# Performance work log

Hardware: AMD Instinct MI355X
Metric: run time of the kernel (lower is better)

## Reference

```python
import jax, jax.numpy as jnp
import numpy as np

B, I, H = 16384, 512, 512


def setup_inputs() -> dict:
    key = jax.random.key(0)
    ks = jax.random.split(key, 6)
    scale_s = 1.0 / np.sqrt(H + I + 1)
    scale_g = 1.0 / np.sqrt(H + I + H)
    return {
        "x_t": jax.random.normal(ks[0], (B, I), dtype=jnp.float32),
        "delta_t": jax.random.uniform(ks[1], (B, 1), dtype=jnp.float32),
        "h_prev": jax.random.normal(ks[2], (B, H), dtype=jnp.float32),
        "c_prev": jax.random.normal(ks[3], (B, H), dtype=jnp.float32),
        # linear_s: in = H + I + 1
        "Ws": jax.random.normal(ks[4], (H + I + 1, H), dtype=jnp.float32) * scale_s,
        "bs": jnp.zeros((H,), dtype=jnp.float32),
        # stacked weights for the 5 gates (f, i, T, u, o), each in = H + I + H
        "Wg": jax.random.normal(ks[5], (2 * H + I, 5 * H), dtype=jnp.float32) * scale_g,
        "bg": jnp.zeros((5 * H,), dtype=jnp.float32),
    }


def reference(x_t, delta_t, h_prev, c_prev, Ws, bs, Wg, bg):
    # time gate: s_t = tanh(Linear([h_prev, x_t, delta_t]))
    s_t = jnp.tanh(jnp.concatenate([h_prev, x_t, delta_t], axis=1) @ Ws + bs)
    # shared-input GEMM for the 5 gates on concat([h_prev, x_t, s_t])
    z = jnp.concatenate([h_prev, x_t, s_t], axis=1) @ Wg + bg  # [B, 5H]
    f_t = jax.nn.sigmoid(z[:, 0 * H:1 * H])
    i_t = jax.nn.sigmoid(z[:, 1 * H:2 * H])
    T_t = jax.nn.sigmoid(z[:, 2 * H:3 * H])
    zeta_t = jnp.tanh(z[:, 3 * H:4 * H])
    o_t = jax.nn.sigmoid(z[:, 4 * H:5 * H])
    c_t = f_t * c_prev + i_t * zeta_t + T_t * s_t
    h_t = o_t * jnp.tanh(c_t)
    return (h_t, c_t)
```

## Files before the change

### kernel.cpp

```cpp
#include <hip/hip_runtime.h>
#include <stdint.h>
#include <stddef.h>

#define Bsz 16384
#define Hsz 512
#define KG 1536
#define KA 1024
#define NT2 24

typedef float f32x4 __attribute__((ext_vector_type(4)));
typedef short bf16x8 __attribute__((ext_vector_type(8)));
typedef unsigned short u16;
typedef unsigned int u32;

__device__ __forceinline__ u16 f2bf(float f) {
  union { float f; unsigned u; } v; v.f = f;
  return (u16)((v.u + 0x7fffu + ((v.u >> 16) & 1u)) >> 16);
}
__device__ __forceinline__ float bf2f(u16 h) {
  union { unsigned u; float f; } v; v.u = ((unsigned)h) << 16;
  return v.f;
}
__device__ __forceinline__ float sigm(float x) {
  return 1.0f / (1.0f + __expf(-x));
}
__device__ __forceinline__ float tanh_(float x) {
  x = fminf(fmaxf(x, -15.0f), 15.0f);
  float e = __expf(2.0f * x);
  return (e - 1.0f) / (e + 1.0f);
}

__device__ __forceinline__ void gload_lds16(const u16* g, u16* l) {
  __builtin_amdgcn_global_load_lds(
      (__attribute__((address_space(1))) void*)(g),
      (__attribute__((address_space(3))) void*)(l), 16, 0, 0);
}

#define VMCNT(n) asm volatile("s_waitcnt vmcnt(" #n ")" ::: "memory")
#define BAR() { asm volatile("" ::: "memory"); __builtin_amdgcn_s_barrier(); \
                asm volatile("" ::: "memory"); }

__global__ __launch_bounds__(256) void prep_A_kernel(
    const float* __restrict__ h_prev, const float* __restrict__ x_t,
    u16* __restrict__ A) {
  const int b = blockIdx.x;
  const int q = threadIdx.x;
  const int qq = q & 127;
  const float4* src = (q < 128) ? (const float4*)h_prev : (const float4*)x_t;
  float4 v = src[(size_t)b * 128 + qq];
  ushort4 o;
  o.x = f2bf(v.x); o.y = f2bf(v.y); o.z = f2bf(v.z); o.w = f2bf(v.w);
  *(ushort4*)(A + (size_t)b * KG + (size_t)q * 4) = o;
}

__global__ __launch_bounds__(256) void transpose_cast_kernel(
    const float* __restrict__ in, u16* __restrict__ out, int R, int C) {
  __shared__ float tile[32][33];
  const int c0 = blockIdx.x * 32;
  const int r0 = blockIdx.y * 32;
  const int tx = threadIdx.x;
  const int ty = threadIdx.y;
  #pragma unroll
  for (int i = ty; i < 32; i += 8)
    tile[i][tx] = in[(size_t)(r0 + i) * C + (c0 + tx)];
  __syncthreads();
  #pragma unroll
  for (int i = ty; i < 32; i += 8)
    out[(size_t)(c0 + i) * R + (r0 + tx)] = f2bf(tile[tx][i]);
}

__global__ __launch_bounds__(256, 2) void gemm1_kernel(
    const u16* __restrict__ A, const u16* __restrict__ Wst,
    const float* __restrict__ Ws, const float* __restrict__ bs,
    const float* __restrict__ delta, u16* __restrict__ Aout) {
  __shared__ __attribute__((aligned(16))) u16 Als[128][32];
  __shared__ __attribute__((aligned(16))) u16 Bls[128][32];
  const int t = threadIdx.x;
  const int w = t >> 6, l = t & 63;
  const int bm0 = blockIdx.y * 128;
  const int bn0 = blockIdx.x * 128;
  const int wm = w >> 1, wn = w & 1;

  f32x4 zv = {0.f, 0.f, 0.f, 0.f};
  f32x4 acc[4][4];
  #pragma unroll
  for (int i = 0; i < 4; ++i)
    #pragma unroll
    for (int j = 0; j < 4; ++j) acc[i][j] = zv;

  const int r = t >> 2, q = t & 3;
  const u16* gA0 = A + (size_t)(bm0 + r) * KG + q * 8;
  const u16* gA1 = A + (size_t)(bm0 + 64 + r) * KG + q * 8;
  const u16* gB0 = Wst + (size_t)(bn0 + r) * KA + q * 8;
  const u16* gB1 = Wst + (size_t)(bn0 + 64 + r) * KA + q * 8;
  u16* lA0 = &Als[0][0] + w * 512;
  u16* lA1 = &Als[0][0] + 2048 + w * 512;
  u16* lB0 = &Bls[0][0] + w * 512;
  u16* lB1 = &Bls[0][0] + 2048 + w * 512;

  const int frow = l & 15;
  const int kofs = (l >> 4) * 8;

  for (int kt = 0; kt < KA / 32; ++kt) {
    const int ko = kt * 32;
    gload_lds16(gA0 + ko, lA0);
    gload_lds16(gA1 + ko, lA1);
    gload_lds16(gB0 + ko, lB0);
    gload_lds16(gB1 + ko, lB1);
    __syncthreads();
    bf16x8 af[4], bfv[4];
    #pragma unroll
    for (int mi = 0; mi < 4; ++mi)
      af[mi] = *(const bf16x8*)&Als[wm * 64 + mi * 16 + frow][kofs];
    #pragma unroll
    for (int ni = 0; ni < 4; ++ni)
      bfv[ni] = *(const bf16x8*)&Bls[wn * 64 + ni * 16 + frow][kofs];
    #pragma unroll
    for (int mi = 0; mi < 4; ++mi)
      #pragma unroll
      for (int ni = 0; ni < 4; ++ni)
        acc[mi][ni] = __builtin_amdgcn_mfma_f32_16x16x32_bf16(
            af[mi], bfv[ni], acc[mi][ni], 0, 0, 0);
    __syncthreads();
  }

  #pragma unroll
  for (int ni = 0; ni < 4; ++ni) {
    const int col = bn0 + wn * 64 + ni * 16 + (l & 15);
    const float wsl = Ws[(size_t)1024 * 512 + col];
    const float bsv = bs[col];
    #pragma unroll
    for (int mi = 0; mi < 4; ++mi) {
      #pragma unroll
      for (int rr = 0; rr < 4; ++rr) {
        const int row = bm0 + wm * 64 + mi * 16 + (l >> 4) * 4 + rr;
        const float z = acc[mi][ni][rr] + delta[row] * wsl + bsv;
        Aout[(size_t)row * KG + 1024 + col] = f2bf(tanh_(z));
      }
    }
  }
}

__global__ __launch_bounds__(512, 2) void gemm2_8ph(
    const u16* __restrict__ A, const u16* __restrict__ Wgt,
    const float* __restrict__ bg, const float* __restrict__ c_prev,
    float* __restrict__ out) {
  __shared__ __attribute__((aligned(16))) u16 LDSA[2][256 * 64];
  __shared__ __attribute__((aligned(16))) u16 LDSB[2][320 * 64];

  const int t5 = threadIdx.x;
  const int w = t5 >> 6;
  const int l = t5 & 63;

  const int bid = blockIdx.x;
  const int hb = bid & 7;
  const int rb = bid >> 3;
  const int bm0 = rb * 256;
  const int h0 = hb * 64;

  const bool isA = (w < 4);

  const int lrow = l >> 3, lch = l & 7;
  const size_t laneoff = (size_t)lrow * KG + (size_t)((lch ^ lrow) * 8);

  const u16* gbase = isA ? (A + (size_t)(bm0 + w * 64) * KG + laneoff)
                         : (Wgt + (size_t)h0 * KG + laneoff);
  u32 boff[10];
  #pragma unroll
  for (int s = 0; s < 10; ++s) {
    int rB = (w - 4) * 80 + s * 8;
    boff[s] = (u32)(((rB >> 6) * Hsz + (rB & 63)) * KG);
  }

#define STAGE(kt) { const u32 _ko = (u32)(kt) * 64; const int _b = (kt) & 1; \
    if (isA) { \
      u16* lb = &LDSA[_b][0] + w * 4096; \
      _Pragma("unroll") \
      for (int s = 0; s < 8; ++s) \
        gload_lds16(gbase + _ko + s * (8 * KG), lb + s * 512); \
    } else { \
      u16* lb = &LDSB[_b][0] + (w - 4) * 5120; \
      _Pragma("unroll") \
      for (int s = 0; s < 10; ++s) \
        gload_lds16(gbase + _ko + boff[s], lb + s * 512); \
    } }

  f32x4 zv = {0.f, 0.f, 0.f, 0.f};
  f32x4 acc[8][5];
  #pragma unroll
  for (int mi = 0; mi < 8; ++mi)
    #pragma unroll
    for (int g = 0; g < 5; ++g) acc[mi][g] = zv;

  const int wm = w >> 2;
  const int wn = w & 3;
  const int frow = l & 15;
  const int kq = l >> 4;
  const int f7 = frow & 7;
  const u32 abase  = (u32)((wm * 128 + frow) * 64 + ((kq ^ f7) * 8));
  const u32 bbase  = (u32)((wn * 16 + frow) * 64 + ((kq ^ f7) * 8));
  const u32 abase2 = abase ^ 32;
  const u32 bbase2 = bbase ^ 32;

#define LDA4(Asrc, off) { af[0] = *(const bf16x8*)&Asrc[(off)]; \
    af[1] = *(const bf16x8*)&Asrc[(off) + 1024]; \
    af[2] = *(const bf16x8*)&Asrc[(off) + 2048]; \
    af[3] = *(const bf16x8*)&Asrc[(off) + 3072]; }
#define LDB5(Bsrc, off) { bfv[0] = *(const bf16x8*)&Bsrc[(off)]; \
    bfv[1] = *(const bf16x8*)&Bsrc[(off) + 4096]; \
    bfv[2] = *(const bf16x8*)&Bsrc[(off) + 8192]; \
    bfv[3] = *(const bf16x8*)&Bsrc[(off) + 12288]; \
    bfv[4] = *(const bf16x8*)&Bsrc[(off) + 16384]; }
#define MFMA20(base) { __builtin_amdgcn_s_setprio(1); \
    _Pragma("unroll") \
    for (int g = 0; g < 5; ++g) { \
      _Pragma("unroll") \
      for (int mi = 0; mi < 4; ++mi) \
        acc[(base) + mi][g] = __builtin_amdgcn_mfma_f32_16x16x32_bf16( \
            af[mi], bfv[g], acc[(base) + mi][g], 0, 0, 0); \
    } \
    __builtin_amdgcn_s_setprio(0); }

  STAGE(0) STAGE(1)

  for (int t = 0; t < NT2; ++t) {
    const int rem = NT2 - 1 - t;
    if (rem >= 1) { VMCNT(8); } else { VMCNT(0); }
    BAR();
    const u16* As = &LDSA[t & 1][0];
    const u16* Bs = &LDSB[t & 1][0];
    bf16x8 af[4], bfv[5];
    LDA4(As, abase) LDB5(Bs, bbase)
    MFMA20(0)
    BAR();
    LDA4(As, abase + 4096)
    MFMA20(4)
    BAR();
    LDA4(As, abase2) LDB5(Bs, bbase2)
    MFMA20(0)
    BAR();
    LDA4(As, abase2 + 4096)
    MFMA20(4)
    BAR();
    if (rem >= 2) STAGE(t + 2)
  }
#undef STAGE

  const int hc = h0 + wn * 16 + frow;
  const float b_f = bg[hc];
  const float b_i = bg[Hsz + hc];
  const float b_T = bg[2 * Hsz + hc];
  const float b_z = bg[3 * Hsz + hc];
  const float b_o = bg[4 * Hsz + hc];
  #pragma unroll
  for (int mi = 0; mi < 8; ++mi) {
    #pragma unroll
    for (int rr = 0; rr < 4; ++rr) {
      const int row = bm0 + wm * 128 + mi * 16 + kq * 4 + rr;
      const float fg = sigm(acc[mi][0][rr] + b_f);
      const float ig = sigm(acc[mi][1][rr] + b_i);
      const float Tg = sigm(acc[mi][2][rr] + b_T);
      const float zg = tanh_(acc[mi][3][rr] + b_z);
      const float og = sigm(acc[mi][4][rr] + b_o);
      const float cp = c_prev[(size_t)row * Hsz + hc];
      const float st = bf2f(A[(size_t)row * KG + 1024 + hc]);
      const float c = fg * cp + ig * zg + Tg * st;
      const float h = og * tanh_(c);
      out[(size_t)row * Hsz + hc] = h;
      out[(size_t)Bsz * Hsz + (size_t)row * Hsz + hc] = c;
    }
  }
}

extern "C" void kernel_launch(void* const* d_in, const int* in_sizes, int n_in,
                              void* d_out, int out_size, void* d_ws, size_t ws_size,
                              hipStream_t stream) {
  const float* x_t    = (const float*)d_in[0];
  const float* delta  = (const float*)d_in[1];
  const float* h_prev = (const float*)d_in[2];
  const float* c_prev = (const float*)d_in[3];
  const float* Ws     = (const float*)d_in[4];
  const float* bs     = (const float*)d_in[5];
  const float* Wg     = (const float*)d_in[6];
  const float* bg     = (const float*)d_in[7];
  float* out = (float*)d_out;

  char* wsb = (char*)d_ws;
  u16* A   = (u16*)(wsb);
  u16* Wst = (u16*)(wsb + (size_t)50331648);
  u16* Wgt = (u16*)(wsb + (size_t)51380224);

  prep_A_kernel<<<dim3(16384), dim3(256), 0, stream>>>(h_prev, x_t, A);
  transpose_cast_kernel<<<dim3(16, 32), dim3(32, 8), 0, stream>>>(Ws, Wst, 1024, 512);
  transpose_cast_kernel<<<dim3(80, 48), dim3(32, 8), 0, stream>>>(Wg, Wgt, 1536, 2560);
  gemm1_kernel<<<dim3(4, 128), dim3(256), 0, stream>>>(A, Wst, Ws, bs, delta, A);
  gemm2_8ph<<<dim3(512), dim3(512), 0, stream>>>(A, Wgt, bg, c_prev, out);
}
```

Before: 211.4 us.

## Load gate-weight fragments directly into registers and triple-buffer A tiles in LDS

The gate GEMM no longer stages the weight tile in shared memory. Each wave loads its B fragments straight from global memory into registers, double-buffered across k-steps. The A tile now uses a three-deep LDS ring with 32-wide k-steps. Inline ds_read plus lgkmcnt waits interleave fragment reads with MFMAs, and there are fewer barriers per step. This removes LDS traffic and LDS capacity for B, but it adds redundant global/L2 reads of the weights across waves and more register pressure.

```diff
diff --git a/kernel.cpp b/kernel.cpp
--- a/kernel.cpp
+++ b/kernel.cpp
@@ -6,7 +6,7 @@
 #define Hsz 512
 #define KG 1536
 #define KA 1024
-#define NT2 24
+#define NT3 48
 
 typedef float f32x4 __attribute__((ext_vector_type(4)));
 typedef short bf16x8 __attribute__((ext_vector_type(8)));
@@ -36,7 +36,15 @@
       (__attribute__((address_space(3))) void*)(l), 16, 0, 0);
 }
 
+__device__ __forceinline__ bf16x8 ds_read128(u32 byte_addr) {
+  bf16x8 r;
+  asm volatile("ds_read_b128 %0, %1" : "=v"(r) : "v"(byte_addr));
+  return r;
+}
+
 #define VMCNT(n) asm volatile("s_waitcnt vmcnt(" #n ")" ::: "memory")
+#define LGKM(n) { asm volatile("s_waitcnt lgkmcnt(" #n ")" ::: "memory"); \
+                  __builtin_amdgcn_sched_barrier(0); }
 #define BAR() { asm volatile("" ::: "memory"); __builtin_amdgcn_s_barrier(); \
                 asm volatile("" ::: "memory"); }
 
@@ -141,12 +149,11 @@
   }
 }
 
-__global__ __launch_bounds__(512, 2) void gemm2_8ph(
+__global__ __launch_bounds__(512, 2) void gemm2_dl(
     const u16* __restrict__ A, const u16* __restrict__ Wgt,
     const float* __restrict__ bg, const float* __restrict__ c_prev,
     float* __restrict__ out) {
-  __shared__ __attribute__((aligned(16))) u16 LDSA[2][256 * 64];
-  __shared__ __attribute__((aligned(16))) u16 LDSB[2][320 * 64];
+  __shared__ __attribute__((aligned(16))) u16 LDSA[3][256 * 32];
 
   const int t5 = threadIdx.x;
   const int w = t5 >> 6;
@@ -158,93 +165,109 @@
   const int bm0 = rb * 256;
   const int h0 = hb * 64;
 
-  const bool isA = (w < 4);
-
-  const int lrow = l >> 3, lch = l & 7;
-  const size_t laneoff = (size_t)lrow * KG + (size_t)((lch ^ lrow) * 8);
-
-  const u16* gbase = isA ? (A + (size_t)(bm0 + w * 64) * KG + laneoff)
-                         : (Wgt + (size_t)h0 * KG + laneoff);
-  u32 boff[10];
-  #pragma unroll
-  for (int s = 0; s < 10; ++s) {
-    int rB = (w - 4) * 80 + s * 8;
-    boff[s] = (u32)(((rB >> 6) * Hsz + (rB & 63)) * KG);
-  }
-
-#define STAGE(kt) { const u32 _ko = (u32)(kt) * 64; const int _b = (kt) & 1; \
-    if (isA) { \
-      u16* lb = &LDSA[_b][0] + w * 4096; \
-      _Pragma("unroll") \
-      for (int s = 0; s < 8; ++s) \
-        gload_lds16(gbase + _ko + s * (8 * KG), lb + s * 512); \
-    } else { \
-      u16* lb = &LDSB[_b][0] + (w - 4) * 5120; \
-      _Pragma("unroll") \
-      for (int s = 0; s < 10; ++s) \
-        gload_lds16(gbase + _ko + boff[s], lb + s * 512); \
-    } }
-
-  f32x4 zv = {0.f, 0.f, 0.f, 0.f};
-  f32x4 acc[8][5];
-  #pragma unroll
-  for (int mi = 0; mi < 8; ++mi)
-    #pragma unroll
-    for (int g = 0; g < 5; ++g) acc[mi][g] = zv;
+  const u16* gsA0; const u16* gsA1;
+  u32 loA0, loA1;
+  {
+    int idx0 = w * 128 + l;
+    int row0 = idx0 >> 2, ch0 = (idx0 & 3) ^ ((idx0 >> 3) & 3);
+    gsA0 = A + (size_t)(bm0 + row0) * KG + ch0 * 8;
+    loA0 = (u32)(w * 128) * 8;
+    int idx1 = w * 128 + 64 + l;
+    int row1 = idx1 >> 2, ch1 = (idx1 & 3) ^ ((idx1 >> 3) & 3);
+    gsA1 = A + (size_t)(bm0 + row1) * KG + ch1 * 8;
+    loA1 = (u32)(w * 128 + 64) * 8;
+  }
 
   const int wm = w >> 2;
   const int wn = w & 3;
   const int frow = l & 15;
   const int kq = l >> 4;
-  const int f7 = frow & 7;
-  const u32 abase  = (u32)((wm * 128 + frow) * 64 + ((kq ^ f7) * 8));
-  const u32 bbase  = (u32)((wn * 16 + frow) * 64 + ((kq ^ f7) * 8));
-  const u32 abase2 = abase ^ 32;
-  const u32 bbase2 = bbase ^ 32;
-
-#define LDA4(Asrc, off) { af[0] = *(const bf16x8*)&Asrc[(off)]; \
-    af[1] = *(const bf16x8*)&Asrc[(off) + 1024]; \
-    af[2] = *(const bf16x8*)&Asrc[(off) + 2048]; \
-    af[3] = *(const bf16x8*)&Asrc[(off) + 3072]; }
-#define LDB5(Bsrc, off) { bfv[0] = *(const bf16x8*)&Bsrc[(off)]; \
-    bfv[1] = *(const bf16x8*)&Bsrc[(off) + 4096]; \
-    bfv[2] = *(const bf16x8*)&Bsrc[(off) + 8192]; \
-    bfv[3] = *(const bf16x8*)&Bsrc[(off) + 12288]; \
-    bfv[4] = *(const bf16x8*)&Bsrc[(off) + 16384]; }
-#define MFMA20(base) { __builtin_amdgcn_s_setprio(1); \
+
+  const u16* barr[5];
+  #pragma unroll
+  for (int g = 0; g < 5; ++g)
+    barr[g] = Wgt + (size_t)(g * Hsz + h0 + wn * 16 + frow) * KG + kq * 8;
+
+  f32x4 zv = {0.f, 0.f, 0.f, 0.f};
+  f32x4 acc[8][5];
+  #pragma unroll
+  for (int mi = 0; mi < 8; ++mi)
+    #pragma unroll
+    for (int g = 0; g < 5; ++g) acc[mi][g] = zv;
+
+  bf16x8 bfvA[5], bfvB[5];
+
+#define GLOADB(DST) { \
     _Pragma("unroll") \
     for (int g = 0; g < 5; ++g) { \
-      _Pragma("unroll") \
-      for (int mi = 0; mi < 4; ++mi) \
-        acc[(base) + mi][g] = __builtin_amdgcn_mfma_f32_16x16x32_bf16( \
-            af[mi], bfv[g], acc[(base) + mi][g], 0, 0, 0); \
+      asm volatile("global_load_dwordx4 %0, %1, off" \
+                   : "=v"(DST[g]) : "v"(barr[g])); \
+      barr[g] += 32; \
+    } }
+
+  const u32 axor = (u32)((kq ^ ((frow >> 1) & 3)) << 3);
+  const u32 abyte = ((u32)(wm * 128 + frow) * 32 + axor) * 2;
+  const u32 ldsA0 = (u32)(uintptr_t)&LDSA[0][0];
+
+#define MFMAG(i0, i1, F0, F1, SRC) { \
+    __builtin_amdgcn_s_setprio(1); \
+    _Pragma("unroll") \
+    for (int g = 0; g < 5; ++g) { \
+      acc[i0][g] = __builtin_amdgcn_mfma_f32_16x16x32_bf16( \
+          F0, SRC[g], acc[i0][g], 0, 0, 0); \
+      acc[i1][g] = __builtin_amdgcn_mfma_f32_16x16x32_bf16( \
+          F1, SRC[g], acc[i1][g], 0, 0, 0); \
     } \
     __builtin_amdgcn_s_setprio(0); }
 
-  STAGE(0) STAGE(1)
-
-  for (int t = 0; t < NT2; ++t) {
-    const int rem = NT2 - 1 - t;
-    if (rem >= 1) { VMCNT(8); } else { VMCNT(0); }
-    BAR();
-    const u16* As = &LDSA[t & 1][0];
-    const u16* Bs = &LDSB[t & 1][0];
-    bf16x8 af[4], bfv[5];
-    LDA4(As, abase) LDB5(Bs, bbase)
-    MFMA20(0)
-    BAR();
-    LDA4(As, abase + 4096)
-    MFMA20(4)
-    BAR();
-    LDA4(As, abase2) LDB5(Bs, bbase2)
-    MFMA20(0)
-    BAR();
-    LDA4(As, abase2 + 4096)
-    MFMA20(4)
-    BAR();
-    if (rem >= 2) STAGE(t + 2)
-  }
-#undef STAGE
+  gload_lds16(gsA0, &LDSA[0][loA0]);
+  gload_lds16(gsA1, &LDSA[0][loA1]);
+  gsA0 += 32; gsA1 += 32;
+  GLOADB(bfvA)
+  gload_lds16(gsA0, &LDSA[1][loA0]);
+  gload_lds16(gsA1, &LDSA[1][loA1]);
+  gsA0 += 32; gsA1 += 32;
+
+  int btA = 0;
+  int btC = 2;
+
+#define TILE_BODY(t, CUR, NXT) { \
+    if ((t) + 1 < NT3) { VMCNT(2); } else { VMCNT(0); } \
+    BAR(); \
+    const u32 aB = ldsA0 + (u32)btA * 16384 + abyte; \
+    bf16x8 af0 = ds_read128(aB); \
+    bf16x8 af1 = ds_read128(aB + 1024); \
+    bf16x8 af2 = ds_read128(aB + 2048); \
+    bf16x8 af3 = ds_read128(aB + 3072); \
+    if ((t) + 1 < NT3) { GLOADB(NXT) } \
+    if ((t) + 2 < NT3) { \
+      gload_lds16(gsA0, &LDSA[btC][loA0]); \
+      gload_lds16(gsA1, &LDSA[btC][loA1]); \
+      gsA0 += 32; gsA1 += 32; \
+    } \
+    bf16x8 af4 = ds_read128(aB + 4096); \
+    bf16x8 af5 = ds_read128(aB + 5120); \
+    LGKM(4)                  \
+    MFMAG(0, 1, af0, af1, CUR) \
+    bf16x8 af6 = ds_read128(aB + 6144); \
+    bf16x8 af7 = ds_read128(aB + 7168); \
+    LGKM(4)                  \
+    MFMAG(2, 3, af2, af3, CUR) \
+    LGKM(2)                  \
+    MFMAG(4, 5, af4, af5, CUR) \
+    LGKM(0)                  \
+    MFMAG(6, 7, af6, af7, CUR) \
+    btA = (btA == 2) ? 0 : btA + 1; \
+    btC = (btC == 2) ? 0 : btC + 1; \
+  }
+
+  for (int t2 = 0; t2 < NT3; t2 += 2) {
+    TILE_BODY(t2, bfvA, bfvB)
+    TILE_BODY(t2 + 1, bfvB, bfvA)
+  }
+#undef TILE_BODY
+#undef GLOADB
+#undef MFMAG
 
   const int hc = h0 + wn * 16 + frow;
   const float b_f = bg[hc];
@@ -294,5 +317,5 @@
   transpose_cast_kernel<<<dim3(16, 32), dim3(32, 8), 0, stream>>>(Ws, Wst, 1024, 512);
   transpose_cast_kernel<<<dim3(80, 48), dim3(32, 8), 0, stream>>>(Wg, Wgt, 1536, 2560);
   gemm1_kernel<<<dim3(4, 128), dim3(256), 0, stream>>>(A, Wst, Ws, bs, delta, A);
-  gemm2_8ph<<<dim3(512), dim3(512), 0, stream>>>(A, Wgt, bg, c_prev, out);
-}
+  gemm2_dl<<<dim3(512), dim3(512), 0, stream>>>(A, Wgt, bg, c_prev, out);
+}
```

After: 241.1 us. +14.0%, slower.

## Restructure gate GEMM main loop with all-wave staging and inline-asm LDS reads

Applied to the files above, without the earlier changes.

Rewrites the main loop of the second GEMM so that all eight waves share the global-to-LDS staging instead of splitting into A-loader and B-loader waves. The next tile's loads are spread across the first two MFMA phases. LDS fragments are read with inline-asm ds_read_b128 using precomputed addresses and immediate offsets under a new swizzle, with explicit lgkmcnt waits and sched barriers. The aim is better overlap of memory loads with MFMA and less address arithmetic, at the cost of a full vmcnt(0) drain and extra barriers per tile.

```diff
diff --git a/kernel.cpp b/kernel.cpp
--- a/kernel.cpp
+++ b/kernel.cpp
@@ -37,8 +37,12 @@
 }
 
 #define VMCNT(n) asm volatile("s_waitcnt vmcnt(" #n ")" ::: "memory")
+#define LGKM0() { asm volatile("s_waitcnt lgkmcnt(0)" ::: "memory"); \
+                  __builtin_amdgcn_sched_barrier(0); }
 #define BAR() { asm volatile("" ::: "memory"); __builtin_amdgcn_s_barrier(); \
                 asm volatile("" ::: "memory"); }
+#define DSR(dst, addr, OFF) \
+  asm volatile("ds_read_b128 %0, %1 offset:" #OFF : "=v"(dst) : "v"(addr));
 
 __global__ __launch_bounds__(256) void prep_A_kernel(
     const float* __restrict__ h_prev, const float* __restrict__ x_t,
@@ -141,110 +145,119 @@
   }
 }
 
-__global__ __launch_bounds__(512, 2) void gemm2_8ph(
+__global__ __launch_bounds__(512, 2) void gemm2_f(
     const u16* __restrict__ A, const u16* __restrict__ Wgt,
     const float* __restrict__ bg, const float* __restrict__ c_prev,
     float* __restrict__ out) {
-  __shared__ __attribute__((aligned(16))) u16 LDSA[2][256 * 64];
-  __shared__ __attribute__((aligned(16))) u16 LDSB[2][320 * 64];
+  __shared__ __attribute__((aligned(16))) u16 LA[2][256 * 64];
+  __shared__ __attribute__((aligned(16))) u16 LB[2][320 * 64];
 
   const int t5 = threadIdx.x;
-  const int w = t5 >> 6;
-  const int l = t5 & 63;
-
+  const int w = t5 >> 6, l = t5 & 63;
   const int bid = blockIdx.x;
   const int hb = bid & 7;
   const int rb = bid >> 3;
   const int bm0 = rb * 256;
   const int h0 = hb * 64;
-
-  const bool isA = (w < 4);
-
-  const int lrow = l >> 3, lch = l & 7;
-  const size_t laneoff = (size_t)lrow * KG + (size_t)((lch ^ lrow) * 8);
-
-  const u16* gbase = isA ? (A + (size_t)(bm0 + w * 64) * KG + laneoff)
-                         : (Wgt + (size_t)h0 * KG + laneoff);
-  u32 boff[10];
-  #pragma unroll
-  for (int s = 0; s < 10; ++s) {
-    int rB = (w - 4) * 80 + s * 8;
-    boff[s] = (u32)(((rB >> 6) * Hsz + (rB & 63)) * KG);
-  }
-
-#define STAGE(kt) { const u32 _ko = (u32)(kt) * 64; const int _b = (kt) & 1; \
-    if (isA) { \
-      u16* lb = &LDSA[_b][0] + w * 4096; \
-      _Pragma("unroll") \
-      for (int s = 0; s < 8; ++s) \
-        gload_lds16(gbase + _ko + s * (8 * KG), lb + s * 512); \
-    } else { \
-      u16* lb = &LDSB[_b][0] + (w - 4) * 5120; \
-      _Pragma("unroll") \
-      for (int s = 0; s < 10; ++s) \
-        gload_lds16(gbase + _ko + boff[s], lb + s * 512); \
-    } }
-
-  f32x4 zv = {0.f, 0.f, 0.f, 0.f};
-  f32x4 acc[8][5];
-  #pragma unroll
-  for (int mi = 0; mi < 8; ++mi)
-    #pragma unroll
-    for (int g = 0; g < 5; ++g) acc[mi][g] = zv;
-
   const int wm = w >> 2;
   const int wn = w & 3;
-  const int frow = l & 15;
-  const int kq = l >> 4;
-  const int f7 = frow & 7;
-  const u32 abase  = (u32)((wm * 128 + frow) * 64 + ((kq ^ f7) * 8));
-  const u32 bbase  = (u32)((wn * 16 + frow) * 64 + ((kq ^ f7) * 8));
-  const u32 abase2 = abase ^ 32;
-  const u32 bbase2 = bbase ^ 32;
-
-#define LDA4(Asrc, off) { af[0] = *(const bf16x8*)&Asrc[(off)]; \
-    af[1] = *(const bf16x8*)&Asrc[(off) + 1024]; \
-    af[2] = *(const bf16x8*)&Asrc[(off) + 2048]; \
-    af[3] = *(const bf16x8*)&Asrc[(off) + 3072]; }
-#define LDB5(Bsrc, off) { bfv[0] = *(const bf16x8*)&Bsrc[(off)]; \
-    bfv[1] = *(const bf16x8*)&Bsrc[(off) + 4096]; \
-    bfv[2] = *(const bf16x8*)&Bsrc[(off) + 8192]; \
-    bfv[3] = *(const bf16x8*)&Bsrc[(off) + 12288]; \
-    bfv[4] = *(const bf16x8*)&Bsrc[(off) + 16384]; }
-#define MFMA20(base) { __builtin_amdgcn_s_setprio(1); \
+
+  const u16* Asrc[4];
+  const u16* Bsrc[5];
+  #pragma unroll
+  for (int j = 0; j < 4; ++j) {
+    u32 d = (u32)(t5 + j * 512) * 16;
+    u32 row = d >> 7;
+    u32 ch = ((d >> 4) & 7) ^ (row & 7);
+    Asrc[j] = A + (size_t)(bm0 + row) * KG + ch * 8;
+  }
+  #pragma unroll
+  for (int j = 0; j < 5; ++j) {
+    u32 d = (u32)(t5 + j * 512) * 16;
+    u32 brow = d >> 7;
+    u32 g = brow >> 6, hl = brow & 63;
+    u32 ch = ((d >> 4) & 7) ^ (brow & 7);
+    Bsrc[j] = Wgt + (size_t)(g * Hsz + h0 + hl) * KG + ch * 8;
+  }
+
+#define STG_A(j, NB, tl) gload_lds16(Asrc[j] + (size_t)(tl) * 64, \
+    &LA[NB][0] + t5 * 8 + (j) * 4096);
+#define STG_B(j, NB, tl) gload_lds16(Bsrc[j] + (size_t)(tl) * 64, \
+    &LB[NB][0] + t5 * 8 + (j) * 4096);
+
+  f32x4 acc[8][5];
+  f32x4 zv = {0.f, 0.f, 0.f, 0.f};
+  #pragma unroll
+  for (int mi = 0; mi < 8; ++mi)
+    #pragma unroll
+    for (int g = 0; g < 5; ++g) acc[mi][g] = zv;
+
+  const int frow = l & 15, kq = l >> 4;
+  const u32 chunk0 = (u32)(((kq ^ (frow & 3)) * 16) + ((frow & 4) * 16));
+  const u32 ldsAb = (u32)(uintptr_t)&LA[0][0];
+  const u32 ldsBb = (u32)(uintptr_t)&LB[0][0];
+  const u32 aK0b0 = ldsAb + (u32)wm * 16384 + (u32)frow * 128 + chunk0;
+  const u32 aK1b0 = aK0b0 ^ 64;
+  const u32 aK0b1 = aK0b0 + 32768;
+  const u32 aK1b1 = aK1b0 + 32768;
+  const u32 bK0b0 = ldsBb + (u32)(wn * 16 + frow) * 128 + chunk0;
+  const u32 bK1b0 = bK0b0 ^ 64;
+  const u32 bK0b1 = bK0b0 + 40960;
+  const u32 bK1b1 = bK1b0 + 40960;
+
+  bf16x8 af0, af1, af2, af3, bf0, bf1, bf2, bf3, bf4;
+
+#define RD_A(AK, MHOFF0, MHOFF1, MHOFF2, MHOFF3) { \
+    DSR(af0, AK, MHOFF0) DSR(af1, AK, MHOFF1) \
+    DSR(af2, AK, MHOFF2) DSR(af3, AK, MHOFF3) }
+#define RD_B(BK) { DSR(bf0, BK, 0) DSR(bf1, BK, 8192) DSR(bf2, BK, 16384) \
+    DSR(bf3, BK, 24576) DSR(bf4, BK, 32768) }
+#define MFMA20(MH) { __builtin_amdgcn_s_setprio(1); \
     _Pragma("unroll") \
     for (int g = 0; g < 5; ++g) { \
-      _Pragma("unroll") \
-      for (int mi = 0; mi < 4; ++mi) \
-        acc[(base) + mi][g] = __builtin_amdgcn_mfma_f32_16x16x32_bf16( \
-            af[mi], bfv[g], acc[(base) + mi][g], 0, 0, 0); \
+      bf16x8 bb = (g == 0) ? bf0 : (g == 1) ? bf1 : (g == 2) ? bf2 \
+                  : (g == 3) ? bf3 : bf4; \
+      acc[(MH) * 4 + 0][g] = __builtin_amdgcn_mfma_f32_16x16x32_bf16(af0, bb, acc[(MH) * 4 + 0][g], 0, 0, 0); \
+      acc[(MH) * 4 + 1][g] = __builtin_amdgcn_mfma_f32_16x16x32_bf16(af1, bb, acc[(MH) * 4 + 1][g], 0, 0, 0); \
+      acc[(MH) * 4 + 2][g] = __builtin_amdgcn_mfma_f32_16x16x32_bf16(af2, bb, acc[(MH) * 4 + 2][g], 0, 0, 0); \
+      acc[(MH) * 4 + 3][g] = __builtin_amdgcn_mfma_f32_16x16x32_bf16(af3, bb, acc[(MH) * 4 + 3][g], 0, 0, 0); \
     } \
     __builtin_amdgcn_s_setprio(0); }
 
-  STAGE(0) STAGE(1)
-
-  for (int t = 0; t < NT2; ++t) {
-    const int rem = NT2 - 1 - t;
-    if (rem >= 1) { VMCNT(8); } else { VMCNT(0); }
-    BAR();
-    const u16* As = &LDSA[t & 1][0];
-    const u16* Bs = &LDSB[t & 1][0];
-    bf16x8 af[4], bfv[5];
-    LDA4(As, abase) LDB5(Bs, bbase)
-    MFMA20(0)
-    BAR();
-    LDA4(As, abase + 4096)
-    MFMA20(4)
-    BAR();
-    LDA4(As, abase2) LDB5(Bs, bbase2)
-    MFMA20(0)
-    BAR();
-    LDA4(As, abase2 + 4096)
-    MFMA20(4)
-    BAR();
-    if (rem >= 2) STAGE(t + 2)
-  }
-#undef STAGE
+#define GROUP(AK0, AK1, BK0, BK1, NB2, tl, st) { \
+     \
+    RD_A(AK0, 0, 2048, 4096, 6144) \
+    RD_B(BK0) \
+    if (st) { STG_A(0, NB2, tl) STG_A(1, NB2, tl) STG_B(0, NB2, tl) STG_B(1, NB2, tl) } \
+    BAR(); LGKM0(); MFMA20(0) BAR(); \
+     \
+    RD_A(AK0, 8192, 10240, 12288, 14336) \
+    if (st) { STG_A(2, NB2, tl) STG_A(3, NB2, tl) STG_B(2, NB2, tl) STG_B(3, NB2, tl) STG_B(4, NB2, tl) } \
+    BAR(); LGKM0(); MFMA20(1) BAR(); \
+     \
+    RD_A(AK1, 0, 2048, 4096, 6144) \
+    RD_B(BK1) \
+    BAR(); LGKM0(); MFMA20(0) BAR(); \
+     \
+    RD_A(AK1, 8192, 10240, 12288, 14336) \
+    BAR(); LGKM0(); MFMA20(1) \
+    VMCNT(0); BAR(); }
+
+  STG_A(0, 0, 0) STG_A(1, 0, 0) STG_A(2, 0, 0) STG_A(3, 0, 0)
+  STG_B(0, 0, 0) STG_B(1, 0, 0) STG_B(2, 0, 0) STG_B(3, 0, 0) STG_B(4, 0, 0)
+  VMCNT(0);
+  BAR();
+
+  for (int j2 = 0; j2 < NT2; j2 += 2) {
+    GROUP(aK0b0, aK1b0, bK0b0, bK1b0, 1, j2 + 1, true)
+    GROUP(aK0b1, aK1b1, bK0b1, bK1b1, 0, j2 + 2, (j2 + 2 < NT2))
+  }
+#undef GROUP
+#undef RD_A
+#undef RD_B
+#undef MFMA20
+#undef STG_A
+#undef STG_B
 
   const int hc = h0 + wn * 16 + frow;
   const float b_f = bg[hc];
@@ -294,5 +307,5 @@
   transpose_cast_kernel<<<dim3(16, 32), dim3(32, 8), 0, stream>>>(Ws, Wst, 1024, 512);
   transpose_cast_kernel<<<dim3(80, 48), dim3(32, 8), 0, stream>>>(Wg, Wgt, 1536, 2560);
   gemm1_kernel<<<dim3(4, 128), dim3(256), 0, stream>>>(A, Wst, Ws, bs, delta, A);
-  gemm2_8ph<<<dim3(512), dim3(512), 0, stream>>>(A, Wgt, bg, c_prev, out);
-}
+  gemm2_f<<<dim3(512), dim3(512), 0, stream>>>(A, Wgt, bg, c_prev, out);
+}
```

Result: slower. 438.5 us (+107.4%).
